# Kernel tuning notes

Hardware: AMD Instinct MI355X
Metric: run time of the kernel (lower is better)

The kernel has to match this reference:

```python
import jax, jax.numpy as jnp
import numpy as np

NODES = 16384
EDGES = 262144
DIM_A, DIM_V, DIM_D, DIM_L = 64, 32, 16, 8
R0 = 8.0

_e = np.zeros((3, 3, 3), dtype=np.float32)
for _i, _j, _k in ((0, 1, 2), (1, 2, 0), (2, 0, 1)):
    _e[_i, _j, _k] = 1.0
    _e[_i, _k, _j] = -1.0
EPS = jnp.asarray(_e)  # Levi-Civita for the antisymmetric (cross-product) couplings


def radial_encode_edge(r, n, rmax):
    """r: (E, 3) -> (E, n) compactly-supported cosine radial basis."""
    npi = jnp.pi * jnp.arange(n, dtype=r.dtype)
    x_sq = (r * r).sum(-1) / rmax
    return jnp.cos(npi * jnp.sqrt(x_sq)[..., None]) * jax.nn.relu(1.0 - x_sq)[..., None]


def tens_sigmoid_vec(x):
    """Equivariant bounded nonlinearity on order-1 tensors (last axis = 3)."""
    n = jnp.linalg.norm(x, axis=-1, keepdims=True)
    return x * jnp.tanh(n) / jnp.maximum(n, 1e-6)


def setup_inputs() -> dict:
    key = jax.random.key(0)
    ks = jax.random.split(key, 24)
    A, V, D, L = DIM_A, DIM_V, DIM_D, DIM_L
    pshapes = {
        "P_000": (A, L, A), "P_110": (A, L, V), "P_220": (A, L, D),
        "P_011": (V, L, V), "P_101": (V, L, A), "P_121": (V, L, D),
        "P_211": (V, L, V), "P_111": (V, L, V),
        "P_022": (D, L, D), "P_112": (D, L, V), "P_202": (D, L, A),
        "P_222": (D, L, D), "P_212": (D, L, V),
    }
    nfac = (L * max(A, V, D)) ** -0.5
    inp = {
        "x_a": jax.random.normal(ks[0], (NODES, A), jnp.float32),
        "x_v": jax.random.normal(ks[1], (NODES, V, 3), jnp.float32),
        "x_d": jax.random.normal(ks[2], (NODES, D, 3, 3), jnp.float32),
        "r_ij": jax.random.normal(ks[3], (EDGES, 3), jnp.float32),
    }
    for i, (name, shp) in enumerate(pshapes.items()):
        inp[name] = jax.random.normal(ks[4 + i], shp, jnp.float32) * nfac
    inp["src"] = jax.random.randint(ks[20], (EDGES,), 0, NODES)
    inp["dst"] = jax.random.randint(ks[21], (EDGES,), 0, NODES)
    return inp


def _forward(x_a, x_v, x_d, r_ij,
             P_000, P_110, P_220, P_011, P_101, P_121, P_211, P_111,
             P_022, P_112, P_202, P_222, P_212, src, dst):
    n_nodes = x_a.shape[0]
    # per-edge radial basis (left operands, dim_l = 8)
    rad = radial_encode_edge(r_ij, DIM_L, R0)              # (E, L)
    rh = tens_sigmoid_vec(r_ij * (7.0 / R0))               # (E, 3)
    phi_a = rad                                            # (E, L)
    phi_v = rad[..., None] * rh[..., None, :]              # (E, L, 3)
    phi_d = rad[..., None, None] * rh[..., None, None, :] * rh[..., None, :, None]  # (E, L, 3, 3)
    # gather node features at edge sources
    xa, xv, xd = x_a[src], x_v[src], x_d[src]
    # CG-style tensor-product contractions P_{left}{right}{out}
    m_a = (jnp.einsum('clb,el,eb->ec', P_000, phi_a, xa)
           + jnp.einsum('clb,eli,ebi->ec', P_110, phi_v, xv)
           + jnp.einsum('clb,elij,ebij->ec', P_220, phi_d, xd))
    m_v = (jnp.einsum('clb,el,ebi->eci', P_011, phi_a, xv)
           + jnp.einsum('clb,eli,eb->eci', P_101, phi_v, xa)
           + jnp.einsum('clb,elj,ebij->eci', P_121, phi_v, xd)
           + jnp.einsum('clb,elij,ebj->eci', P_211, phi_d, xv)
           + jnp.einsum('ijk,clb,elj,ebk->eci', EPS, P_111, phi_v, xv))
    m_d = (jnp.einsum('clb,el,ebij->ecij', P_022, phi_a, xd)
           + jnp.einsum('clb,eli,ebj->ecij', P_112, phi_v, xv)
           + jnp.einsum('clb,elij,eb->ecij', P_202, phi_d, xa)
           + jnp.einsum('clb,elik,ebkj->ecij', P_222, phi_d, xd)
           + jnp.einsum('jkm,clb,elik,ebm->ecij', EPS, P_212, phi_d, xv))
    # scatter-sum messages to destination nodes
    y_a = jax.ops.segment_sum(m_a, dst, num_segments=n_nodes)
    y_v = jax.ops.segment_sum(m_v, dst, num_segments=n_nodes)
    y_d = jax.ops.segment_sum(m_d, dst, num_segments=n_nodes)
    # pack (a, v, d) channels into one array: (N, A + 3V + 9D)
    return jnp.concatenate([y_a, y_v.reshape(n_nodes, -1), y_d.reshape(n_nodes, -1)], axis=-1)


def reference(x_a, x_v, x_d, r_ij,
              P_000, P_110, P_220, P_011, P_101, P_121, P_211, P_111,
              P_022, P_112, P_202, P_222, P_212, src, dst):
    return _forward(x_a, x_v, x_d, r_ij,
                    P_000, P_110, P_220, P_011, P_101, P_121, P_211, P_111,
                    P_022, P_112, P_202, P_222, P_212, src, dst)
```

## Files before the change

### kernel.cpp

```cpp
#include <hip/hip_runtime.h>

#define NODES    16384
#define EDGES    262144
#define OUT_CH   304
#define EB       16
#define NTHREADS 256

typedef __attribute__((ext_vector_type(8))) short short8;
typedef __attribute__((ext_vector_type(4))) float f32x4;
typedef __attribute__((ext_vector_type(8))) float f32x8;
typedef __attribute__((ext_vector_type(8))) __bf16 bf16x8;
#define MFMA(a,b,c) __builtin_amdgcn_mfma_f32_16x16x32_bf16((a),(b),(c),0,0,0)

#define NB1 100352
#define NB2 36864
#define NB3 2048
#define NPACK (NB1 + NB2 + NB3)

__global__ __launch_bounds__(256) void prep_kernel(
    const float* __restrict__ P000, const float* __restrict__ P110, const float* __restrict__ P220,
    const float* __restrict__ P011, const float* __restrict__ P101, const float* __restrict__ P121,
    const float* __restrict__ P211, const float* __restrict__ P111,
    const float* __restrict__ P022, const float* __restrict__ P112, const float* __restrict__ P202,
    const float* __restrict__ P222, const float* __restrict__ P212,
    unsigned short* __restrict__ BP,
    const int* __restrict__ dst, int* __restrict__ cnt)
{
    int idx = blockIdx.x*256 + threadIdx.x;
    if (idx < NPACK) {
        float v = 0.0f;
        if (idx < NB1) {
            int j = idx & 7, lane = (idx >> 3) & 63, q = idx >> 9;
            int tile = q % 7, kk = q / 7;
            int n = tile*16 + (lane & 15);
            int k = kk*32 + (lane >> 4)*8 + j;
            int l = k & 7, b = k >> 3;
            if (n < 64) {           int c = n;
                if      (b <  64) v = P000[(c*8+l)*64 + b];
                else if (b <  96) v = P110[(c*8+l)*32 + (b-64)];
                else              v = P220[(c*8+l)*16 + (b-96)];
            } else if (n < 96) {    int c = n - 64;
                if      (b <  64) v = P101[(c*8+l)*64 + b];
                else if (b <  96) v = P211[(c*8+l)*32 + (b-64)];
            } else {                int c = n - 96;
                if      (b <  64) v = P202[(c*8+l)*64 + b];
            }
        } else if (idx < NB1 + NB2) {
            int o = idx - NB1;
            int j = o & 7, lane = (o >> 3) & 63, q = o >> 9;
            int tile = q % 3, kk = q / 3;
            int n = tile*16 + (lane & 15);
            int k = kk*32 + (lane >> 4)*8 + j;
            int l = k & 7, b = k >> 3;
            if (n < 32) {           int c = n;
                if      (b <  32) v = P011[(c*8+l)*32 + b];
                else if (b <  48) v = P121[(c*8+l)*16 + (b-32)];
                else if (b <  80) v = P111[(c*8+l)*32 + (b-48)];
            } else {                int c = n - 32;
                if      (b <  32) v = P112[(c*8+l)*32 + b];
                else if (b <  48) v = 0.0f;
                else if (b <  80) v = P212[(c*8+l)*32 + (b-48)];
                else              v = P222[(c*8+l)*16 + (b-80)];
            }
        } else {
            int o = idx - NB1 - NB2;
            int j = o & 7, lane = (o >> 3) & 63, kk = o >> 9;
            int n = lane & 15;
            int k = kk*32 + (lane >> 4)*8 + j;
            int l = k & 7, b = k >> 3;
            v = P022[(n*8+l)*16 + b];
        }
        union { float f; unsigned int i; } x; x.f = v;
        unsigned int i = x.i;
        i += 0x7fffu + ((i >> 16) & 1u);
        BP[idx] = (unsigned short)(i >> 16);
    }
    if (idx < EDGES) atomicAdd(&cnt[dst[idx]], 1);
}

__global__ __launch_bounds__(256) void scan_kernel(const int* __restrict__ cnt,
                                                   int* __restrict__ off,
                                                   int* __restrict__ cursor)
{
    __shared__ int s_part[256];
    const int t = threadIdx.x;
    const int base = t * 64;
    int sum = 0;
    for (int i = 0; i < 64; ++i) sum += cnt[base + i];
    s_part[t] = sum;
    __syncthreads();
    for (int d = 1; d < 256; d <<= 1) {
        int add = (t >= d) ? s_part[t - d] : 0;
        __syncthreads();
        s_part[t] += add;
        __syncthreads();
    }
    int run = s_part[t] - sum;
    for (int i = 0; i < 64; ++i) {
        int c = cnt[base + i];
        off[base + i]    = run;
        cursor[base + i] = run;
        run += c;
    }
    if (t == 255) off[NODES] = run;
}

__global__ __launch_bounds__(256) void scatter_kernel(const int* __restrict__ dst,
                                                      int* __restrict__ cursor,
                                                      int* __restrict__ eidx)
{
    int e = blockIdx.x*256 + threadIdx.x;
    if (e < EDGES) {
        int pos = atomicAdd(&cursor[dst[e]], 1);
        eidx[pos] = e;
    }
}

__device__ __forceinline__ short8 build2(const f32x8 radv, float f)
{
    f32x8 z = radv * f;
    bf16x8 zb = __builtin_convertvector(z, bf16x8);
    union { bf16x8 b; short8 s; } w; w.b = zb;
    return w.s;
}

struct FeatPool {
    float FS[EB][116];
    float FVT[EB][3][100];
};
struct MsgPool {
    float m[EB][308];
    float as0[EB][32];
    float a00[EB][16];
    float aj[EB][3][16];
};
union Pool {
    FeatPool f;
    MsgPool  g;
};

__global__ __launch_bounds__(NTHREADS, 4) void edge_kernel(
    const float* __restrict__ xa_g, const float* __restrict__ xv_g, const float* __restrict__ xd_g,
    const float* __restrict__ rij_g,
    const unsigned short* __restrict__ BP,
    const int* __restrict__ src, const int* __restrict__ dst, const int* __restrict__ eidx,
    float* __restrict__ out)
{
    __shared__ __align__(16) Pool s_p;
    __shared__ __align__(16) float s_FDT[EB][9][20];
    __shared__ float s_rad[EB][9];
    __shared__ float s_rh[EB][4];
    __shared__ int   s_dst[EB];
    __shared__ int   s_srcn[EB];

    const int t  = threadIdx.x;
    const int e0 = blockIdx.x * EB;
    const int lane = t & 63, wid = t >> 6;
    const int col = lane & 15, quad = lane >> 4;

    const short8* __restrict__ B1 = (const short8*)BP;
    const short8* __restrict__ B2 = (const short8*)(BP + NB1);
    const short8* __restrict__ B3 = (const short8*)(BP + NB1 + NB2);

    if (t < EB) {
        const int e = eidx[e0 + t];
        float r0 = rij_g[e*3+0];
        float r1 = rij_g[e*3+1];
        float r2 = rij_g[e*3+2];
        float x_sq = (r0*r0 + r1*r1 + r2*r2) * 0.125f;
        float q  = sqrtf(x_sq);
        float w  = fmaxf(1.0f - x_sq, 0.0f);
        const float PI = 3.14159265358979323846f;
        for (int n = 0; n < 8; ++n)
            s_rad[t][n] = cosf(PI * (float)n * q) * w;
        float y0 = r0*0.875f, y1 = r1*0.875f, y2 = r2*0.875f;
        float nn = sqrtf(y0*y0 + y1*y1 + y2*y2);
        float sc = tanhf(nn) / fmaxf(nn, 1e-6f);
        s_rh[t][0] = y0*sc; s_rh[t][1] = y1*sc; s_rh[t][2] = y2*sc; s_rh[t][3] = 0.f;
        s_dst[t]  = dst[e];
        s_srcn[t] = src[e];
    }
    __syncthreads();

    {
        const int el  = t >> 4;
        const int sub = t & 15;
        const int n   = s_srcn[el];
        const float rh0 = s_rh[el][0], rh1 = s_rh[el][1], rh2 = s_rh[el][2];
        #pragma unroll
        for (int k = 0; k < 4; ++k) {
            int b = sub + 16*k;
            s_p.f.FS[el][b] = xa_g[n*64 + b];
        }
        #pragma unroll
        for (int k = 0; k < 2; ++k) {
            int b = sub + 16*k;
            float v0 = xv_g[(n*32 + b)*3 + 0];
            float v1 = xv_g[(n*32 + b)*3 + 1];
            float v2 = xv_g[(n*32 + b)*3 + 2];
            s_p.f.FVT[el][0][b] = v0;
            s_p.f.FVT[el][1][b] = v1;
            s_p.f.FVT[el][2][b] = v2;
            s_p.f.FS[el][64 + b] = rh0*v0 + rh1*v1 + rh2*v2;
            s_p.f.FVT[el][0][48 + b] = rh1*v2 - rh2*v1;
            s_p.f.FVT[el][1][48 + b] = rh2*v0 - rh0*v2;
            s_p.f.FVT[el][2][48 + b] = rh0*v1 - rh1*v0;
        }
        {
            const int b = sub;
            const float d0 = xd_g[(n*16+b)*9+0], d1 = xd_g[(n*16+b)*9+1], d2 = xd_g[(n*16+b)*9+2];
            const float d3 = xd_g[(n*16+b)*9+3], d4 = xd_g[(n*16+b)*9+4], d5 = xd_g[(n*16+b)*9+5];
            const float d6 = xd_g[(n*16+b)*9+6], d7 = xd_g[(n*16+b)*9+7], d8 = xd_g[(n*16+b)*9+8];
            s_FDT[el][0][b]=d0; s_FDT[el][1][b]=d1; s_FDT[el][2][b]=d2;
            s_FDT[el][3][b]=d3; s_FDT[el][4][b]=d4; s_FDT[el][5][b]=d5;
            s_FDT[el][6][b]=d6; s_FDT[el][7][b]=d7; s_FDT[el][8][b]=d8;
            const float uv0 = d0*rh0 + d1*rh1 + d2*rh2;
            const float uv1 = d3*rh0 + d4*rh1 + d5*rh2;
            const float uv2 = d6*rh0 + d7*rh1 + d8*rh2;
            s_p.f.FVT[el][0][32 + b] = uv0;
            s_p.f.FVT[el][1][32 + b] = uv1;
            s_p.f.FVT[el][2][32 + b] = uv2;
            s_p.f.FVT[el][0][80 + b] = rh0*d0 + rh1*d3 + rh2*d6;
            s_p.f.FVT[el][1][80 + b] = rh0*d1 + rh1*d4 + rh2*d7;
            s_p.f.FVT[el][2][80 + b] = rh0*d2 + rh1*d5 + rh2*d8;
            s_p.f.FS[el][96 + b] = rh0*uv0 + rh1*uv1 + rh2*uv2;
        }
    }
    __syncthreads();

    f32x8 radv;
    #pragma unroll
    for (int l = 0; l < 8; ++l) radv[l] = s_rad[col][l];
    const int r0 = quad*4;
    f32x4 R0={0,0,0,0}, R1={0,0,0,0}, R2={0,0,0,0}, R3={0,0,0,0};
    f32x4 R4={0,0,0,0}, R5={0,0,0,0}, R6={0,0,0,0}, R7={0,0,0,0};

    if (wid == 0) {
        const float* frow = &s_p.f.FS[col][0];
        for (int kk = 0; kk < 28; ++kk) {
            short8 a = build2(radv, frow[kk*4 + quad]);
            const short8* bp = B1 + (kk*7)*64 + lane;
            R0 = MFMA(a, bp[0*64], R0);
            R1 = MFMA(a, bp[1*64], R1);
            R2 = MFMA(a, bp[2*64], R2);
            R3 = MFMA(a, bp[3*64], R3);
        }
        #pragma unroll
        for (int kk = 0; kk < 4; ++kk) {
            const int kq = kk*4 + quad;
            const short8 b3 = B3[kk*64 + lane];
            R4 = MFMA(build2(radv, s_FDT[col][0][kq]), b3, R4);
            R5 = MFMA(build2(radv, s_FDT[col][1][kq]), b3, R5);
            R6 = MFMA(build2(radv, s_FDT[col][2][kq]), b3, R6);
            R7 = MFMA(build2(radv, s_FDT[col][3][kq]), b3, R7);
        }
    } else if (wid == 1) {
        const float* frow = &s_p.f.FS[col][0];
        for (int kk = 0; kk < 28; ++kk) {
            short8 a = build2(radv, frow[kk*4 + quad]);
            const short8* bp = B1 + (kk*7)*64 + lane;
            R0 = MFMA(a, bp[4*64], R0);
            R1 = MFMA(a, bp[5*64], R1);
            R2 = MFMA(a, bp[6*64], R2);
        }
        #pragma unroll
        for (int kk = 0; kk < 4; ++kk) {
            const int kq = kk*4 + quad;
            const short8 b3 = B3[kk*64 + lane];
            R3 = MFMA(build2(radv, s_FDT[col][4][kq]), b3, R3);
            R4 = MFMA(build2(radv, s_FDT[col][5][kq]), b3, R4);
            R5 = MFMA(build2(radv, s_FDT[col][6][kq]), b3, R5);
            R6 = MFMA(build2(radv, s_FDT[col][7][kq]), b3, R6);
            R7 = MFMA(build2(radv, s_FDT[col][8][kq]), b3, R7);
        }
    } else if (wid == 2) {
        const float* f0 = &s_p.f.FVT[col][0][0];
        const float* f1 = &s_p.f.FVT[col][1][0];
        for (int kk = 0; kk < 24; ++kk) {
            const int kq = kk*4 + quad;
            short8 a0 = build2(radv, f0[kq]);
            short8 a1 = build2(radv, f1[kq]);
            const short8* bp = B2 + (kk*3)*64 + lane;
            short8 b0 = bp[0*64], b1 = bp[1*64], b2 = bp[2*64];
            R0 = MFMA(a0, b0, R0);
            R1 = MFMA(a0, b1, R1);
            R2 = MFMA(a0, b2, R2);
            R3 = MFMA(a1, b0, R3);
            R4 = MFMA(a1, b1, R4);
        }
    } else {
        const float* f1 = &s_p.f.FVT[col][1][0];
        const float* f2 = &s_p.f.FVT[col][2][0];
        for (int kk = 0; kk < 24; ++kk) {
            const int kq = kk*4 + quad;
            short8 a1 = build2(radv, f1[kq]);
            short8 a2 = build2(radv, f2[kq]);
            const short8* bp = B2 + (kk*3)*64 + lane;
            short8 b0 = bp[0*64], b1 = bp[1*64], b2 = bp[2*64];
            R0 = MFMA(a1, b2, R0);
            R1 = MFMA(a2, b0, R1);
            R2 = MFMA(a2, b1, R2);
            R3 = MFMA(a2, b2, R3);
        }
    }
    __syncthreads();

    if (wid == 0) {
        #pragma unroll
        for (int r = 0; r < 4; ++r) {
            s_p.g.m[r0+r][ 0+col] = R0[r];
            s_p.g.m[r0+r][16+col] = R1[r];
            s_p.g.m[r0+r][32+col] = R2[r];
            s_p.g.m[r0+r][48+col] = R3[r];
            s_p.g.m[r0+r][160 + col*9 + 0] = R4[r];
            s_p.g.m[r0+r][160 + col*9 + 1] = R5[r];
            s_p.g.m[r0+r][160 + col*9 + 2] = R6[r];
            s_p.g.m[r0+r][160 + col*9 + 3] = R7[r];
        }
    } else if (wid == 1) {
        #pragma unroll
        for (int r = 0; r < 4; ++r) {
            s_p.g.as0[r0+r][ 0+col] = R0[r];
            s_p.g.as0[r0+r][16+col] = R1[r];
            s_p.g.a00[r0+r][col]    = R2[r];
            s_p.g.m[r0+r][160 + col*9 + 4] = R3[r];
            s_p.g.m[r0+r][160 + col*9 + 5] = R4[r];
            s_p.g.m[r0+r][160 + col*9 + 6] = R5[r];
            s_p.g.m[r0+r][160 + col*9 + 7] = R6[r];
            s_p.g.m[r0+r][160 + col*9 + 8] = R7[r];
        }
    } else if (wid == 2) {
        #pragma unroll
        for (int r = 0; r < 4; ++r) {
            s_p.g.m[r0+r][64 + ( 0+col)*3 + 0] = R0[r];
            s_p.g.m[r0+r][64 + (16+col)*3 + 0] = R1[r];
            s_p.g.aj[r0+r][0][col]             = R2[r];
            s_p.g.m[r0+r][64 + ( 0+col)*3 + 1] = R3[r];
            s_p.g.m[r0+r][64 + (16+col)*3 + 1] = R4[r];
        }
    } else {
        #pragma unroll
        for (int r = 0; r < 4; ++r) {
            s_p.g.aj[r0+r][1][col]             = R0[r];
            s_p.g.m[r0+r][64 + ( 0+col)*3 + 2] = R1[r];
            s_p.g.m[r0+r][64 + (16+col)*3 + 2] = R2[r];
            s_p.g.aj[r0+r][2][col]             = R3[r];
        }
    }
    __syncthreads();

    #pragma unroll
    for (int it = t; it < EB*32; it += NTHREADS) {
        const int el = it >> 5, c = it & 31;
        const float as0 = s_p.g.as0[el][c];
        s_p.g.m[el][64 + c*3 + 0] += s_rh[el][0]*as0;
        s_p.g.m[el][64 + c*3 + 1] += s_rh[el][1]*as0;
        s_p.g.m[el][64 + c*3 + 2] += s_rh[el][2]*as0;
    }
    {
        const int el = t >> 4, c = t & 15;
        const float a00 = s_p.g.a00[el][c];
        const float aj0 = s_p.g.aj[el][0][c], aj1 = s_p.g.aj[el][1][c], aj2 = s_p.g.aj[el][2][c];
        const float rr0 = s_rh[el][0], rr1 = s_rh[el][1], rr2 = s_rh[el][2];
        const float g0 = aj0 + rr0*a00, g1 = aj1 + rr1*a00, g2 = aj2 + rr2*a00;
        float* md = &s_p.g.m[el][160 + c*9];
        md[0] += rr0*g0; md[1] += rr0*g1; md[2] += rr0*g2;
        md[3] += rr1*g0; md[4] += rr1*g1; md[5] += rr1*g2;
        md[6] += rr2*g0; md[7] += rr2*g1; md[8] += rr2*g2;
    }
    __syncthreads();

    for (int ch = t; ch < OUT_CH; ch += NTHREADS) {
        float run = 0.0f;
        #pragma unroll
        for (int el = 0; el < EB; ++el) {
            run += s_p.g.m[el][ch];
            if (el == EB-1 || s_dst[el+1] != s_dst[el]) {
                atomicAdd(&out[(size_t)s_dst[el]*OUT_CH + ch], run);
                run = 0.0f;
            }
        }
    }
}

extern "C" void kernel_launch(void* const* d_in, const int* in_sizes, int n_in,
                              void* d_out, int out_size, void* d_ws, size_t ws_size,
                              hipStream_t stream)
{
    const float* xa  = (const float*)d_in[0];
    const float* xv  = (const float*)d_in[1];
    const float* xd  = (const float*)d_in[2];
    const float* rij = (const float*)d_in[3];
    const float* P000 = (const float*)d_in[4];
    const float* P110 = (const float*)d_in[5];
    const float* P220 = (const float*)d_in[6];
    const float* P011 = (const float*)d_in[7];
    const float* P101 = (const float*)d_in[8];
    const float* P121 = (const float*)d_in[9];
    const float* P211 = (const float*)d_in[10];
    const float* P111 = (const float*)d_in[11];
    const float* P022 = (const float*)d_in[12];
    const float* P112 = (const float*)d_in[13];
    const float* P202 = (const float*)d_in[14];
    const float* P222 = (const float*)d_in[15];
    const float* P212 = (const float*)d_in[16];
    const int* src = (const int*)d_in[17];
    const int* dst = (const int*)d_in[18];

    unsigned short* BP = (unsigned short*)d_ws;
    int* ip     = (int*)d_ws + (NPACK/2);
    int* cnt    = ip;
    int* off    = ip + NODES;
    int* cursor = off + NODES + 1;
    int* eidx   = cursor + NODES;

    hipMemsetAsync(cnt, 0, NODES * sizeof(int), stream);
    hipMemsetAsync(d_out, 0, (size_t)out_size * sizeof(float), stream);

    prep_kernel<<<EDGES/256, 256, 0, stream>>>(
        P000, P110, P220, P011, P101, P121, P211, P111,
        P022, P112, P202, P222, P212, BP, dst, cnt);
    scan_kernel   <<<1,         256, 0, stream>>>(cnt, off, cursor);
    scatter_kernel<<<EDGES/256, 256, 0, stream>>>(dst, cursor, eidx);

    edge_kernel<<<EDGES/EB, NTHREADS, 0, stream>>>(
        xa, xv, xd, rij, BP, src, dst, eidx, (float*)d_out);
}
```

Before: 407.6 us.

## Double edges per block and redistribute MFMA work across eight waves

The edge kernel now handles 32 edges per block with 512 threads. Each wave computes two 16-edge MFMA tiles that share one B-operand load, so each weight fragment is reused across twice as many edges, and the output tiles are rebalanced over eight waves. The scan kernel also moves from 256 to 1024 threads, shortening each thread's serial loop. The cost is more registers and shared memory per block, which may lower occupancy.

```diff
diff --git a/kernel.cpp b/kernel.cpp
--- a/kernel.cpp
+++ b/kernel.cpp
@@ -3,8 +3,8 @@
 #define NODES    16384
 #define EDGES    262144
 #define OUT_CH   304
-#define EB       16
-#define NTHREADS 256
+#define EB       32
+#define NTHREADS 512
 
 typedef __attribute__((ext_vector_type(8))) short short8;
 typedef __attribute__((ext_vector_type(4))) float f32x4;
@@ -78,31 +78,31 @@
     if (idx < EDGES) atomicAdd(&cnt[dst[idx]], 1);
 }
 
-__global__ __launch_bounds__(256) void scan_kernel(const int* __restrict__ cnt,
-                                                   int* __restrict__ off,
-                                                   int* __restrict__ cursor)
-{
-    __shared__ int s_part[256];
+__global__ __launch_bounds__(1024) void scan_kernel(const int* __restrict__ cnt,
+                                                    int* __restrict__ off,
+                                                    int* __restrict__ cursor)
+{
+    __shared__ int s_part[1024];
     const int t = threadIdx.x;
-    const int base = t * 64;
+    const int base = t * 16;
     int sum = 0;
-    for (int i = 0; i < 64; ++i) sum += cnt[base + i];
+    for (int i = 0; i < 16; ++i) sum += cnt[base + i];
     s_part[t] = sum;
     __syncthreads();
-    for (int d = 1; d < 256; d <<= 1) {
+    for (int d = 1; d < 1024; d <<= 1) {
         int add = (t >= d) ? s_part[t - d] : 0;
         __syncthreads();
         s_part[t] += add;
         __syncthreads();
     }
     int run = s_part[t] - sum;
-    for (int i = 0; i < 64; ++i) {
+    for (int i = 0; i < 16; ++i) {
         int c = cnt[base + i];
         off[base + i]    = run;
         cursor[base + i] = run;
         run += c;
     }
-    if (t == 255) off[NODES] = run;
+    if (t == 1023) off[NODES] = run;
 }
 
 __global__ __launch_bounds__(256) void scatter_kernel(const int* __restrict__ dst,
@@ -228,123 +228,190 @@
     }
     __syncthreads();
 
-    f32x8 radv;
+    f32x8 radv_lo, radv_hi;
     #pragma unroll
-    for (int l = 0; l < 8; ++l) radv[l] = s_rad[col][l];
+    for (int l = 0; l < 8; ++l) { radv_lo[l] = s_rad[col][l]; radv_hi[l] = s_rad[16+col][l]; }
     const int r0 = quad*4;
-    f32x4 R0={0,0,0,0}, R1={0,0,0,0}, R2={0,0,0,0}, R3={0,0,0,0};
-    f32x4 R4={0,0,0,0}, R5={0,0,0,0}, R6={0,0,0,0}, R7={0,0,0,0};
-
-    if (wid == 0) {
-        const float* frow = &s_p.f.FS[col][0];
+    f32x4 A0={0,0,0,0}, A1={0,0,0,0}, A2={0,0,0,0}, A3={0,0,0,0}, A4={0,0,0,0};
+    f32x4 A5={0,0,0,0}, A6={0,0,0,0}, A7={0,0,0,0}, A8={0,0,0,0}, A9={0,0,0,0};
+
+    if (wid < 3) {
+        const int Ta = wid*2, Tb = wid*2 + 1;
         for (int kk = 0; kk < 28; ++kk) {
-            short8 a = build2(radv, frow[kk*4 + quad]);
+            short8 al = build2(radv_lo, s_p.f.FS[col][kk*4 + quad]);
+            short8 ah = build2(radv_hi, s_p.f.FS[16+col][kk*4 + quad]);
             const short8* bp = B1 + (kk*7)*64 + lane;
-            R0 = MFMA(a, bp[0*64], R0);
-            R1 = MFMA(a, bp[1*64], R1);
-            R2 = MFMA(a, bp[2*64], R2);
-            R3 = MFMA(a, bp[3*64], R3);
+            short8 bA = bp[Ta*64], bB = bp[Tb*64];
+            A0 = MFMA(al, bA, A0);  A1 = MFMA(ah, bA, A1);
+            A2 = MFMA(al, bB, A2);  A3 = MFMA(ah, bB, A3);
+        }
+    } else if (wid == 3) {
+        for (int kk = 0; kk < 28; ++kk) {
+            short8 al = build2(radv_lo, s_p.f.FS[col][kk*4 + quad]);
+            short8 ah = build2(radv_hi, s_p.f.FS[16+col][kk*4 + quad]);
+            short8 b = B1[(kk*7 + 6)*64 + lane];
+            A0 = MFMA(al, b, A0);  A1 = MFMA(ah, b, A1);
+        }
+        for (int kk = 0; kk < 24; ++kk) {
+            short8 al = build2(radv_lo, s_p.f.FVT[col][2][kk*4 + quad]);
+            short8 ah = build2(radv_hi, s_p.f.FVT[16+col][2][kk*4 + quad]);
+            short8 b = B2[(kk*3 + 0)*64 + lane];
+            A2 = MFMA(al, b, A2);  A3 = MFMA(ah, b, A3);
+        }
+    } else if (wid == 4) {
+        for (int kk = 0; kk < 24; ++kk) {
+            short8 al = build2(radv_lo, s_p.f.FVT[col][0][kk*4 + quad]);
+            short8 ah = build2(radv_hi, s_p.f.FVT[16+col][0][kk*4 + quad]);
+            const short8* bp = B2 + (kk*3)*64 + lane;
+            short8 b0 = bp[0*64], b1 = bp[1*64];
+            A0 = MFMA(al, b0, A0);  A1 = MFMA(ah, b0, A1);
+            A2 = MFMA(al, b1, A2);  A3 = MFMA(ah, b1, A3);
         }
         #pragma unroll
         for (int kk = 0; kk < 4; ++kk) {
-            const int kq = kk*4 + quad;
-            const short8 b3 = B3[kk*64 + lane];
-            R4 = MFMA(build2(radv, s_FDT[col][0][kq]), b3, R4);
-            R5 = MFMA(build2(radv, s_FDT[col][1][kq]), b3, R5);
-            R6 = MFMA(build2(radv, s_FDT[col][2][kq]), b3, R6);
-            R7 = MFMA(build2(radv, s_FDT[col][3][kq]), b3, R7);
-        }
-    } else if (wid == 1) {
-        const float* frow = &s_p.f.FS[col][0];
-        for (int kk = 0; kk < 28; ++kk) {
-            short8 a = build2(radv, frow[kk*4 + quad]);
-            const short8* bp = B1 + (kk*7)*64 + lane;
-            R0 = MFMA(a, bp[4*64], R0);
-            R1 = MFMA(a, bp[5*64], R1);
-            R2 = MFMA(a, bp[6*64], R2);
+            short8 b = B3[kk*64 + lane];
+            A4 = MFMA(build2(radv_lo, s_FDT[col][0][kk*4+quad]), b, A4);
+            A5 = MFMA(build2(radv_hi, s_FDT[16+col][0][kk*4+quad]), b, A5);
+            A6 = MFMA(build2(radv_lo, s_FDT[col][1][kk*4+quad]), b, A6);
+            A7 = MFMA(build2(radv_hi, s_FDT[16+col][1][kk*4+quad]), b, A7);
+            A8 = MFMA(build2(radv_lo, s_FDT[col][2][kk*4+quad]), b, A8);
+            A9 = MFMA(build2(radv_hi, s_FDT[16+col][2][kk*4+quad]), b, A9);
+        }
+    } else if (wid == 5) {
+        for (int kk = 0; kk < 24; ++kk) {
+            short8 a0l = build2(radv_lo, s_p.f.FVT[col][0][kk*4 + quad]);
+            short8 a0h = build2(radv_hi, s_p.f.FVT[16+col][0][kk*4 + quad]);
+            short8 a1l = build2(radv_lo, s_p.f.FVT[col][1][kk*4 + quad]);
+            short8 a1h = build2(radv_hi, s_p.f.FVT[16+col][1][kk*4 + quad]);
+            const short8* bp = B2 + (kk*3)*64 + lane;
+            short8 b2 = bp[2*64], b0 = bp[0*64];
+            A0 = MFMA(a0l, b2, A0);  A1 = MFMA(a0h, b2, A1);
+            A2 = MFMA(a1l, b0, A2);  A3 = MFMA(a1h, b0, A3);
         }
         #pragma unroll
         for (int kk = 0; kk < 4; ++kk) {
-            const int kq = kk*4 + quad;
-            const short8 b3 = B3[kk*64 + lane];
-            R3 = MFMA(build2(radv, s_FDT[col][4][kq]), b3, R3);
-            R4 = MFMA(build2(radv, s_FDT[col][5][kq]), b3, R4);
-            R5 = MFMA(build2(radv, s_FDT[col][6][kq]), b3, R5);
-            R6 = MFMA(build2(radv, s_FDT[col][7][kq]), b3, R6);
-            R7 = MFMA(build2(radv, s_FDT[col][8][kq]), b3, R7);
-        }
-    } else if (wid == 2) {
-        const float* f0 = &s_p.f.FVT[col][0][0];
-        const float* f1 = &s_p.f.FVT[col][1][0];
+            short8 b = B3[kk*64 + lane];
+            A4 = MFMA(build2(radv_lo, s_FDT[col][3][kk*4+quad]), b, A4);
+            A5 = MFMA(build2(radv_hi, s_FDT[16+col][3][kk*4+quad]), b, A5);
+            A6 = MFMA(build2(radv_lo, s_FDT[col][4][kk*4+quad]), b, A6);
+            A7 = MFMA(build2(radv_hi, s_FDT[16+col][4][kk*4+quad]), b, A7);
+        }
+    } else if (wid == 6) {
         for (int kk = 0; kk < 24; ++kk) {
-            const int kq = kk*4 + quad;
-            short8 a0 = build2(radv, f0[kq]);
-            short8 a1 = build2(radv, f1[kq]);
+            short8 al = build2(radv_lo, s_p.f.FVT[col][1][kk*4 + quad]);
+            short8 ah = build2(radv_hi, s_p.f.FVT[16+col][1][kk*4 + quad]);
             const short8* bp = B2 + (kk*3)*64 + lane;
-            short8 b0 = bp[0*64], b1 = bp[1*64], b2 = bp[2*64];
-            R0 = MFMA(a0, b0, R0);
-            R1 = MFMA(a0, b1, R1);
-            R2 = MFMA(a0, b2, R2);
-            R3 = MFMA(a1, b0, R3);
-            R4 = MFMA(a1, b1, R4);
+            short8 b1 = bp[1*64], b2 = bp[2*64];
+            A0 = MFMA(al, b1, A0);  A1 = MFMA(ah, b1, A1);
+            A2 = MFMA(al, b2, A2);  A3 = MFMA(ah, b2, A3);
+        }
+        #pragma unroll
+        for (int kk = 0; kk < 4; ++kk) {
+            short8 b = B3[kk*64 + lane];
+            A4 = MFMA(build2(radv_lo, s_FDT[col][5][kk*4+quad]), b, A4);
+            A5 = MFMA(build2(radv_hi, s_FDT[16+col][5][kk*4+quad]), b, A5);
+            A6 = MFMA(build2(radv_lo, s_FDT[col][6][kk*4+quad]), b, A6);
+            A7 = MFMA(build2(radv_hi, s_FDT[16+col][6][kk*4+quad]), b, A7);
         }
     } else {
-        const float* f1 = &s_p.f.FVT[col][1][0];
-        const float* f2 = &s_p.f.FVT[col][2][0];
         for (int kk = 0; kk < 24; ++kk) {
-            const int kq = kk*4 + quad;
-            short8 a1 = build2(radv, f1[kq]);
-            short8 a2 = build2(radv, f2[kq]);
+            short8 al = build2(radv_lo, s_p.f.FVT[col][2][kk*4 + quad]);
+            short8 ah = build2(radv_hi, s_p.f.FVT[16+col][2][kk*4 + quad]);
             const short8* bp = B2 + (kk*3)*64 + lane;
-            short8 b0 = bp[0*64], b1 = bp[1*64], b2 = bp[2*64];
-            R0 = MFMA(a1, b2, R0);
-            R1 = MFMA(a2, b0, R1);
-            R2 = MFMA(a2, b1, R2);
-            R3 = MFMA(a2, b2, R3);
-        }
-    }
-    __syncthreads();
-
-    if (wid == 0) {
-        #pragma unroll
-        for (int r = 0; r < 4; ++r) {
-            s_p.g.m[r0+r][ 0+col] = R0[r];
-            s_p.g.m[r0+r][16+col] = R1[r];
-            s_p.g.m[r0+r][32+col] = R2[r];
-            s_p.g.m[r0+r][48+col] = R3[r];
-            s_p.g.m[r0+r][160 + col*9 + 0] = R4[r];
-            s_p.g.m[r0+r][160 + col*9 + 1] = R5[r];
-            s_p.g.m[r0+r][160 + col*9 + 2] = R6[r];
-            s_p.g.m[r0+r][160 + col*9 + 3] = R7[r];
-        }
-    } else if (wid == 1) {
-        #pragma unroll
-        for (int r = 0; r < 4; ++r) {
-            s_p.g.as0[r0+r][ 0+col] = R0[r];
-            s_p.g.as0[r0+r][16+col] = R1[r];
-            s_p.g.a00[r0+r][col]    = R2[r];
-            s_p.g.m[r0+r][160 + col*9 + 4] = R3[r];
-            s_p.g.m[r0+r][160 + col*9 + 5] = R4[r];
-            s_p.g.m[r0+r][160 + col*9 + 6] = R5[r];
-            s_p.g.m[r0+r][160 + col*9 + 7] = R6[r];
-            s_p.g.m[r0+r][160 + col*9 + 8] = R7[r];
-        }
-    } else if (wid == 2) {
-        #pragma unroll
-        for (int r = 0; r < 4; ++r) {
-            s_p.g.m[r0+r][64 + ( 0+col)*3 + 0] = R0[r];
-            s_p.g.m[r0+r][64 + (16+col)*3 + 0] = R1[r];
-            s_p.g.aj[r0+r][0][col]             = R2[r];
-            s_p.g.m[r0+r][64 + ( 0+col)*3 + 1] = R3[r];
-            s_p.g.m[r0+r][64 + (16+col)*3 + 1] = R4[r];
+            short8 b1 = bp[1*64], b2 = bp[2*64];
+            A0 = MFMA(al, b1, A0);  A1 = MFMA(ah, b1, A1);
+            A2 = MFMA(al, b2, A2);  A3 = MFMA(ah, b2, A3);
+        }
+        #pragma unroll
+        for (int kk = 0; kk < 4; ++kk) {
+            short8 b = B3[kk*64 + lane];
+            A4 = MFMA(build2(radv_lo, s_FDT[col][7][kk*4+quad]), b, A4);
+            A5 = MFMA(build2(radv_hi, s_FDT[16+col][7][kk*4+quad]), b, A5);
+            A6 = MFMA(build2(radv_lo, s_FDT[col][8][kk*4+quad]), b, A6);
+            A7 = MFMA(build2(radv_hi, s_FDT[16+col][8][kk*4+quad]), b, A7);
+        }
+    }
+    __syncthreads();
+
+    if (wid < 3) {
+        const int Ta = wid*2, Tb = wid*2 + 1;
+        #pragma unroll
+        for (int r = 0; r < 4; ++r) {
+            const int elo = r0+r, ehi = 16+r0+r;
+            if (wid < 2) {
+                s_p.g.m[elo][Ta*16+col] = A0[r];
+                s_p.g.m[ehi][Ta*16+col] = A1[r];
+                s_p.g.m[elo][Tb*16+col] = A2[r];
+                s_p.g.m[ehi][Tb*16+col] = A3[r];
+            } else {
+                s_p.g.as0[elo][col]    = A0[r];
+                s_p.g.as0[ehi][col]    = A1[r];
+                s_p.g.as0[elo][16+col] = A2[r];
+                s_p.g.as0[ehi][16+col] = A3[r];
+            }
+        }
+    } else if (wid == 3) {
+        #pragma unroll
+        for (int r = 0; r < 4; ++r) {
+            const int elo = r0+r, ehi = 16+r0+r;
+            s_p.g.a00[elo][col] = A0[r];
+            s_p.g.a00[ehi][col] = A1[r];
+            s_p.g.m[elo][64 + col*3 + 2] = A2[r];
+            s_p.g.m[ehi][64 + col*3 + 2] = A3[r];
+        }
+    } else if (wid == 4) {
+        #pragma unroll
+        for (int r = 0; r < 4; ++r) {
+            const int elo = r0+r, ehi = 16+r0+r;
+            s_p.g.m[elo][64 + col*3 + 0]      = A0[r];
+            s_p.g.m[ehi][64 + col*3 + 0]      = A1[r];
+            s_p.g.m[elo][64 + (16+col)*3 + 0] = A2[r];
+            s_p.g.m[ehi][64 + (16+col)*3 + 0] = A3[r];
+            s_p.g.m[elo][160 + col*9 + 0] = A4[r];
+            s_p.g.m[ehi][160 + col*9 + 0] = A5[r];
+            s_p.g.m[elo][160 + col*9 + 1] = A6[r];
+            s_p.g.m[ehi][160 + col*9 + 1] = A7[r];
+            s_p.g.m[elo][160 + col*9 + 2] = A8[r];
+            s_p.g.m[ehi][160 + col*9 + 2] = A9[r];
+        }
+    } else if (wid == 5) {
+        #pragma unroll
+        for (int r = 0; r < 4; ++r) {
+            const int elo = r0+r, ehi = 16+r0+r;
+            s_p.g.aj[elo][0][col] = A0[r];
+            s_p.g.aj[ehi][0][col] = A1[r];
+            s_p.g.m[elo][64 + col*3 + 1] = A2[r];
+            s_p.g.m[ehi][64 + col*3 + 1] = A3[r];
+            s_p.g.m[elo][160 + col*9 + 3] = A4[r];
+            s_p.g.m[ehi][160 + col*9 + 3] = A5[r];
+            s_p.g.m[elo][160 + col*9 + 4] = A6[r];
+            s_p.g.m[ehi][160 + col*9 + 4] = A7[r];
+        }
+    } else if (wid == 6) {
+        #pragma unroll
+        for (int r = 0; r < 4; ++r) {
+            const int elo = r0+r, ehi = 16+r0+r;
+            s_p.g.m[elo][64 + (16+col)*3 + 1] = A0[r];
+            s_p.g.m[ehi][64 + (16+col)*3 + 1] = A1[r];
+            s_p.g.aj[elo][1][col] = A2[r];
+            s_p.g.aj[ehi][1][col] = A3[r];
+            s_p.g.m[elo][160 + col*9 + 5] = A4[r];
+            s_p.g.m[ehi][160 + col*9 + 5] = A5[r];
+            s_p.g.m[elo][160 + col*9 + 6] = A6[r];
+            s_p.g.m[ehi][160 + col*9 + 6] = A7[r];
         }
     } else {
         #pragma unroll
         for (int r = 0; r < 4; ++r) {
-            s_p.g.aj[r0+r][1][col]             = R0[r];
-            s_p.g.m[r0+r][64 + ( 0+col)*3 + 2] = R1[r];
-            s_p.g.m[r0+r][64 + (16+col)*3 + 2] = R2[r];
-            s_p.g.aj[r0+r][2][col]             = R3[r];
+            const int elo = r0+r, ehi = 16+r0+r;
+            s_p.g.m[elo][64 + (16+col)*3 + 2] = A0[r];
+            s_p.g.m[ehi][64 + (16+col)*3 + 2] = A1[r];
+            s_p.g.aj[elo][2][col] = A2[r];
+            s_p.g.aj[ehi][2][col] = A3[r];
+            s_p.g.m[elo][160 + col*9 + 7] = A4[r];
+            s_p.g.m[ehi][160 + col*9 + 7] = A5[r];
+            s_p.g.m[elo][160 + col*9 + 8] = A6[r];
+            s_p.g.m[ehi][160 + col*9 + 8] = A7[r];
         }
     }
     __syncthreads();
@@ -420,7 +487,7 @@
     prep_kernel<<<EDGES/256, 256, 0, stream>>>(
         P000, P110, P220, P011, P101, P121, P211, P111,
         P022, P112, P202, P222, P212, BP, dst, cnt);
-    scan_kernel   <<<1,         256, 0, stream>>>(cnt, off, cursor);
+    scan_kernel   <<<1,        1024, 0, stream>>>(cnt, off, cursor);
     scatter_kernel<<<EDGES/256, 256, 0, stream>>>(dst, cursor, eidx);
 
     edge_kernel<<<EDGES/EB, NTHREADS, 0, stream>>>(
```

New measurement: 374.5 us. -8.1%, faster.
